# Optimization experiments

Hardware: AMD Instinct MI355X
Metric: run time of the kernel (lower is better)

## Reference

```python
import jax, jax.numpy as jnp
import numpy as np

B = 16384      # batch
H = 1024       # latent_dim
C = 2          # output_dim (classes)
PPC = 24       # prototypes per class
P = C * PPC    # 48 total prototypes
EPS = 1e-4


def setup_inputs() -> dict:
    key = jax.random.key(0)
    k1, k2, k3, k4, k5 = jax.random.split(key, 5)
    specific_user = jax.random.normal(k1, (B, H), jnp.float32)
    shared_user = jax.random.normal(k2, (B, H), jnp.float32)
    prototype_vectors = jax.random.normal(k3, (P, H), jnp.float32)
    # last_layer weight set by set_last_layer_incorrect_connection(-0.5):
    # +1 for the prototype's own class, -0.5 elsewhere; shape [C, P]
    cls = np.arange(P) // PPC
    ident = (cls[None, :] == np.arange(C)[:, None]).astype(np.float32)
    last_layer_w = jnp.asarray(ident * 1.0 + (1.0 - ident) * (-0.5))
    # nn.Bilinear(H, H, 1): weight [1, H, H], bias [1]
    bilinear_w = jax.random.normal(k4, (1, H, H), jnp.float32) / np.sqrt(H)
    bilinear_b = jax.random.normal(k5, (1,), jnp.float32) * 0.01
    return {
        "specific_user": specific_user,
        "shared_user": shared_user,
        "prototype_vectors": prototype_vectors,
        "last_layer_w": last_layer_w,
        "bilinear_w": bilinear_w,
        "bilinear_b": bilinear_b,
        "flag": 1,
    }


def reference(specific_user, shared_user, prototype_vectors, last_layer_w,
              bilinear_w, bilinear_b, flag):
    # prototype_distances: squared euclid via mm + norms, then log-similarity
    x2 = jnp.sum(specific_user ** 2, axis=1, keepdims=True)          # [B,1]
    p2 = jnp.sum(prototype_vectors ** 2, axis=1)                     # [P]
    distance = -2.0 * (specific_user @ prototype_vectors.T) + x2 + p2[None, :]  # [B,P]
    similarity = jnp.log((distance + 1.0) / (distance + EPS))        # [B,P]
    logits = similarity @ last_layer_w.T                             # [B,C]

    # select the class's 24 prototypes (flag picks class 1 or 0; static int)
    idx = 1 if flag else 0
    sub = prototype_vectors.reshape(C, PPC, H)[idx]                  # [PPC,H]

    # prototype_subgraph_distances: per original broadcast, each row of
    # all_sim is the batch-mean of the log-similarity -> constant over batch.
    s2 = jnp.sum(sub ** 2, axis=1)                                   # [PPC]
    d = -2.0 * (specific_user @ sub.T) + x2 + s2[None, :]            # [B,PPC]
    sim = jnp.mean(jnp.log((d + 1.0) / (d + EPS)), axis=0)           # [PPC]
    jstar = jnp.argmax(sim)                                          # scalar
    chosen_proto = jnp.broadcast_to(sub[jstar], specific_user.shape) # [B,H]

    # nn.Bilinear(chosen_proto, shared_user) -> [B,1]
    pos = jnp.einsum('bi,ij,bj->b', chosen_proto, bilinear_w[0], shared_user)[:, None] + bilinear_b
    return (pos, shared_user, logits, distance)
```

## Files before the change

kernel.cpp:

```cpp
#include <hip/hip_runtime.h>
#include <hip/hip_bf16.h>

#define BATCH 16384
#define HD    1024
#define NP    48
#define PPC   24
#define EPSV  1e-4f

typedef __attribute__((ext_vector_type(8))) short  short8;
typedef __attribute__((ext_vector_type(4))) float  floatx4;

__device__ __forceinline__ float b2f(unsigned short s) {
    union { unsigned u; float f; } c; c.u = ((unsigned)s) << 16; return c.f;
}
__device__ __forceinline__ unsigned short f2bu(float f) {
    __hip_bfloat16 h = __float2bfloat16(f);
    union { __hip_bfloat16 h; unsigned short u; } c; c.h = h; return c.u;
}

__global__ __launch_bounds__(256) void k_prep(const float* __restrict__ proto,
                                              unsigned short* __restrict__ phi,
                                              unsigned short* __restrict__ plo,
                                              float* __restrict__ p2,
                                              float* __restrict__ vzero,
                                              float* __restrict__ gcol) {
    const int p = blockIdx.x;
    const int tid = threadIdx.x;
    if (p < 4)                        vzero[p * 256 + tid] = 0.f;
    else if (p == 4 && tid < NP)      gcol[tid] = 0.f;

    const float* row = proto + (size_t)p * HD;
    float acc = 0.f;
#pragma unroll
    for (int c = 0; c < 4; ++c) {
        const int k = c * 256 + tid;
        const float f = row[k];
        acc += f * f;
        const unsigned short h = f2bu(f);
        phi[(size_t)p * HD + k] = h;
        plo[(size_t)p * HD + k] = f2bu(f - b2f(h));
    }
#pragma unroll
    for (int m = 32; m >= 1; m >>= 1) acc += __shfl_xor(acc, m, 64);
    __shared__ float wsum[4];
    if ((tid & 63) == 0) wsum[tid >> 6] = acc;
    __syncthreads();
    if (tid == 0) p2[p] = wsum[0] + wsum[1] + wsum[2] + wsum[3];
}

__global__ __launch_bounds__(256, 4) void k_mainA(
    const float* __restrict__ x,
    const unsigned short* __restrict__ phi,
    const unsigned short* __restrict__ plo,
    float* __restrict__ dotp,
    float* __restrict__ x2h)
{
    __shared__ float lacc[4][64][13];
    __shared__ float lx2[4][16];
    const int wave = threadIdx.x >> 6;
    const int lane = threadIdx.x & 63;
    const int quad = lane >> 4;
    const int lr   = lane & 15;
    const int band = blockIdx.x >> 1;
    const int kh   = blockIdx.x & 1;
    const int rb   = band * 16;
    const int ko   = kh * 512 + wave * 128;

    const float* xr = x + (size_t)(rb + lr) * HD + ko + quad * 8;
    const unsigned short* ph0 = phi + (size_t)lr * HD + ko + quad * 8;
    const unsigned short* ph1 = ph0 + 16 * HD;
    const unsigned short* ph2 = ph0 + 32 * HD;
    const unsigned short* pl0 = plo + (size_t)lr * HD + ko + quad * 8;
    const unsigned short* pl1 = pl0 + 16 * HD;
    const unsigned short* pl2 = pl0 + 32 * HD;

    floatx4 acc0 = {0.f, 0.f, 0.f, 0.f};
    floatx4 acc1 = {0.f, 0.f, 0.f, 0.f};
    floatx4 acc2 = {0.f, 0.f, 0.f, 0.f};
    float x2p = 0.f;

#pragma unroll 2
    for (int kk = 0; kk < 4; ++kk) {
        const floatx4 xa = *(const floatx4*)(xr + kk * 32);
        const floatx4 xb = *(const floatx4*)(xr + kk * 32 + 4);
        short8 ah, al;
#pragma unroll
        for (int j = 0; j < 4; ++j) {
            const float f = xa[j];
            x2p += f * f;
            const unsigned short h = f2bu(f);
            ah[j] = (short)h;
            al[j] = (short)f2bu(f - b2f(h));
        }
#pragma unroll
        for (int j = 0; j < 4; ++j) {
            const float f = xb[j];
            x2p += f * f;
            const unsigned short h = f2bu(f);
            ah[4 + j] = (short)h;
            al[4 + j] = (short)f2bu(f - b2f(h));
        }
        const short8 bh0 = *(const short8*)(ph0 + kk * 32);
        const short8 bh1 = *(const short8*)(ph1 + kk * 32);
        const short8 bh2 = *(const short8*)(ph2 + kk * 32);
        const short8 bl0 = *(const short8*)(pl0 + kk * 32);
        const short8 bl1 = *(const short8*)(pl1 + kk * 32);
        const short8 bl2 = *(const short8*)(pl2 + kk * 32);
        acc0 = __builtin_amdgcn_mfma_f32_16x16x32_bf16(ah, bh0, acc0, 0, 0, 0);
        acc0 = __builtin_amdgcn_mfma_f32_16x16x32_bf16(ah, bl0, acc0, 0, 0, 0);
        acc0 = __builtin_amdgcn_mfma_f32_16x16x32_bf16(al, bh0, acc0, 0, 0, 0);
        acc1 = __builtin_amdgcn_mfma_f32_16x16x32_bf16(ah, bh1, acc1, 0, 0, 0);
        acc1 = __builtin_amdgcn_mfma_f32_16x16x32_bf16(ah, bl1, acc1, 0, 0, 0);
        acc1 = __builtin_amdgcn_mfma_f32_16x16x32_bf16(al, bh1, acc1, 0, 0, 0);
        acc2 = __builtin_amdgcn_mfma_f32_16x16x32_bf16(ah, bh2, acc2, 0, 0, 0);
        acc2 = __builtin_amdgcn_mfma_f32_16x16x32_bf16(ah, bl2, acc2, 0, 0, 0);
        acc2 = __builtin_amdgcn_mfma_f32_16x16x32_bf16(al, bh2, acc2, 0, 0, 0);
    }
    x2p += __shfl_xor(x2p, 16, 64);
    x2p += __shfl_xor(x2p, 32, 64);

#pragma unroll
    for (int r = 0; r < 4; ++r) {
        lacc[wave][lane][r]     = acc0[r];
        lacc[wave][lane][4 + r] = acc1[r];
        lacc[wave][lane][8 + r] = acc2[r];
    }
    if (quad == 0) lx2[wave][lr] = x2p;
    __syncthreads();
    if (wave != 0) return;

    float facc[12];
#pragma unroll
    for (int i = 0; i < 12; ++i)
        facc[i] = lacc[0][lane][i] + lacc[1][lane][i] + lacc[2][lane][i] + lacc[3][lane][i];
    const float x2full = lx2[0][lr] + lx2[1][lr] + lx2[2][lr] + lx2[3][lr];

    float* drow = dotp + ((size_t)kh * 1024 + band) * (16 * NP);
#pragma unroll
    for (int t = 0; t < 3; ++t)
#pragma unroll
        for (int r = 0; r < 4; ++r)
            drow[(quad * 4 + r) * NP + t * 16 + lr] = facc[t * 4 + r];
    if (quad == 0) x2h[((size_t)kh * 1024 + band) * 16 + lr] = x2full;
}

__global__ __launch_bounds__(256) void k_fin(
    const float* __restrict__ dotp,
    const float* __restrict__ x2h,
    const float* __restrict__ p2,
    const float* __restrict__ llw,
    float* __restrict__ gcol,
    float* __restrict__ out_logits,
    float* __restrict__ out_dist)
{
    __shared__ float gsum[NP];
    const int wave = threadIdx.x >> 6;
    const int lane = threadIdx.x & 63;
    const int band = blockIdx.x;
    if (threadIdx.x < NP) gsum[threadIdx.x] = 0.f;
    __syncthreads();

    const float p2p = (lane < NP) ? p2[lane] : 0.f;
    const float w0  = (lane < NP) ? llw[lane] : 0.f;
    const float w1  = (lane < NP) ? llw[NP + lane] : 0.f;
    const float* dA = dotp + (size_t)band * (16 * NP);
    const float* dB = dotp + ((size_t)1024 + band) * (16 * NP);
    float csum = 0.f;

#pragma unroll
    for (int r = 0; r < 4; ++r) {
        const int rrow = wave * 4 + r;
        const int row  = band * 16 + rrow;
        const float x2 = x2h[band * 16 + rrow] + x2h[1024 * 16 + band * 16 + rrow];
        float sim = 0.f;
        if (lane < NP) {
            const float dot = dA[rrow * NP + lane] + dB[rrow * NP + lane];
            const float d = -2.f * dot + x2 + p2p;
            out_dist[(size_t)row * NP + lane] = d;
            sim = log1pf((1.f - EPSV) / (d + EPSV));
        }
        csum += sim;
        float r0 = sim * w0, r1 = sim * w1;
#pragma unroll
        for (int m = 1; m <= 32; m <<= 1) {
            r0 += __shfl_xor(r0, m, 64);
            r1 += __shfl_xor(r1, m, 64);
        }
        if (lane == 0) {
            out_logits[(size_t)row * 2 + 0] = r0;
            out_logits[(size_t)row * 2 + 1] = r1;
        }
    }
    if (lane < NP) atomicAdd(&gsum[lane], csum);
    __syncthreads();
    if (threadIdx.x < NP) atomicAdd(&gcol[threadIdx.x], gsum[threadIdx.x]);
}

__global__ __launch_bounds__(256, 4) void k_main_fb(
    const float* __restrict__ x,
    const unsigned short* __restrict__ phi,
    const unsigned short* __restrict__ plo,
    const float* __restrict__ llw,
    const float* __restrict__ p2,
    float* __restrict__ gcol,
    float* __restrict__ out_logits,
    float* __restrict__ out_dist)
{
    __shared__ float lacc[4][64][13];
    __shared__ float lx2[4][16];
    const int wave = threadIdx.x >> 6;
    const int lane = threadIdx.x & 63;
    const int quad = lane >> 4;
    const int lr   = lane & 15;
    const int rb   = blockIdx.x * 16;
    const int ko   = wave * 256;

    const float* xr = x + (size_t)(rb + lr) * HD + ko + quad * 8;
    const unsigned short* ph0 = phi + (size_t)lr * HD + ko + quad * 8;
    const unsigned short* ph1 = ph0 + 16 * HD;
    const unsigned short* ph2 = ph0 + 32 * HD;
    const unsigned short* pl0 = plo + (size_t)lr * HD + ko + quad * 8;
    const unsigned short* pl1 = pl0 + 16 * HD;
    const unsigned short* pl2 = pl0 + 32 * HD;

    floatx4 acc0 = {0.f, 0.f, 0.f, 0.f};
    floatx4 acc1 = {0.f, 0.f, 0.f, 0.f};
    floatx4 acc2 = {0.f, 0.f, 0.f, 0.f};
    float x2p = 0.f;

#pragma unroll 2
    for (int kk = 0; kk < 8; ++kk) {
        const floatx4 xa = *(const floatx4*)(xr + kk * 32);
        const floatx4 xb = *(const floatx4*)(xr + kk * 32 + 4);
        short8 ah, al;
#pragma unroll
        for (int j = 0; j < 4; ++j) {
            const float f = xa[j];
            x2p += f * f;
            const unsigned short h = f2bu(f);
            ah[j] = (short)h;
            al[j] = (short)f2bu(f - b2f(h));
        }
#pragma unroll
        for (int j = 0; j < 4; ++j) {
            const float f = xb[j];
            x2p += f * f;
            const unsigned short h = f2bu(f);
            ah[4 + j] = (short)h;
            al[4 + j] = (short)f2bu(f - b2f(h));
        }
        const short8 bh0 = *(const short8*)(ph0 + kk * 32);
        const short8 bh1 = *(const short8*)(ph1 + kk * 32);
        const short8 bh2 = *(const short8*)(ph2 + kk * 32);
        const short8 bl0 = *(const short8*)(pl0 + kk * 32);
        const short8 bl1 = *(const short8*)(pl1 + kk * 32);
        const short8 bl2 = *(const short8*)(pl2 + kk * 32);
        acc0 = __builtin_amdgcn_mfma_f32_16x16x32_bf16(ah, bh0, acc0, 0, 0, 0);
        acc0 = __builtin_amdgcn_mfma_f32_16x16x32_bf16(ah, bl0, acc0, 0, 0, 0);
        acc0 = __builtin_amdgcn_mfma_f32_16x16x32_bf16(al, bh0, acc0, 0, 0, 0);
        acc1 = __builtin_amdgcn_mfma_f32_16x16x32_bf16(ah, bh1, acc1, 0, 0, 0);
        acc1 = __builtin_amdgcn_mfma_f32_16x16x32_bf16(ah, bl1, acc1, 0, 0, 0);
        acc1 = __builtin_amdgcn_mfma_f32_16x16x32_bf16(al, bh1, acc1, 0, 0, 0);
        acc2 = __builtin_amdgcn_mfma_f32_16x16x32_bf16(ah, bh2, acc2, 0, 0, 0);
        acc2 = __builtin_amdgcn_mfma_f32_16x16x32_bf16(ah, bl2, acc2, 0, 0, 0);
        acc2 = __builtin_amdgcn_mfma_f32_16x16x32_bf16(al, bh2, acc2, 0, 0, 0);
    }
    x2p += __shfl_xor(x2p, 16, 64);
    x2p += __shfl_xor(x2p, 32, 64);

#pragma unroll
    for (int r = 0; r < 4; ++r) {
        lacc[wave][lane][r]     = acc0[r];
        lacc[wave][lane][4 + r] = acc1[r];
        lacc[wave][lane][8 + r] = acc2[r];
    }
    if (quad == 0) lx2[wave][lr] = x2p;
    __syncthreads();
    if (wave != 0) return;

    float facc[12];
#pragma unroll
    for (int i = 0; i < 12; ++i)
        facc[i] = lacc[0][lane][i] + lacc[1][lane][i] + lacc[2][lane][i] + lacc[3][lane][i];
    const float x2full = lx2[0][lr] + lx2[1][lr] + lx2[2][lr] + lx2[3][lr];

    float s0[4] = {0.f, 0.f, 0.f, 0.f};
    float s1[4] = {0.f, 0.f, 0.f, 0.f};

#pragma unroll
    for (int t = 0; t < 3; ++t) {
        const int p = t * 16 + lr;
        const float p2p = p2[p];
        const float w0 = llw[p];
        const float w1 = llw[NP + p];
        float cst = 0.f;
#pragma unroll
        for (int r = 0; r < 4; ++r) {
            const int row = quad * 4 + r;
            const float x2r = __shfl(x2full, row, 64);
            const float d = -2.f * facc[t * 4 + r] + x2r + p2p;
            out_dist[(size_t)(rb + row) * NP + p] = d;
            const float sim = log1pf((1.f - EPSV) / (d + EPSV));
            s0[r] += sim * w0;
            s1[r] += sim * w1;
            cst += sim;
        }
        cst += __shfl_xor(cst, 16, 64);
        cst += __shfl_xor(cst, 32, 64);
        if (quad == 0) atomicAdd(&gcol[p], cst);
    }

#pragma unroll
    for (int r = 0; r < 4; ++r) {
        float r0 = s0[r], r1 = s1[r];
#pragma unroll
        for (int m = 1; m <= 8; m <<= 1) {
            r0 += __shfl_xor(r0, m, 64);
            r1 += __shfl_xor(r1, m, 64);
        }
        if (lr == 0) {
            const int brow = rb + quad * 4 + r;
            out_logits[(size_t)brow * 2 + 0] = r0;
            out_logits[(size_t)brow * 2 + 1] = r1;
        }
    }
}

__global__ __launch_bounds__(256) void k_matvec(
    const float* __restrict__ proto,
    const float* __restrict__ w2,
    const float* __restrict__ gcol,
    const int* __restrict__ flag,
    float* __restrict__ v)
{
    __shared__ int js;
    const int tid = threadIdx.x;
    const int idx = (flag[0] != 0) ? 1 : 0;
    if (tid == 0) {
        const float* cs = gcol + idx * PPC;
        int bj = 0; float bv = cs[0];
        for (int j = 1; j < PPC; ++j)
            if (cs[j] > bv) { bv = cs[j]; bj = j; }
        js = bj;
    }
    __syncthreads();

    const float* crow = proto + (size_t)(idx * PPC + js) * HD;
    const int i0 = blockIdx.x * 16;
    const int j4 = tid * 4;
    float a0 = 0.f, a1 = 0.f, a2 = 0.f, a3 = 0.f;
#pragma unroll 4
    for (int i = i0; i < i0 + 16; ++i) {
        const float c = crow[i];
        const floatx4 wv = *(const floatx4*)(w2 + (size_t)i * HD + j4);
        a0 += c * wv[0];
        a1 += c * wv[1];
        a2 += c * wv[2];
        a3 += c * wv[3];
    }
    atomicAdd(&v[j4 + 0], a0);
    atomicAdd(&v[j4 + 1], a1);
    atomicAdd(&v[j4 + 2], a2);
    atomicAdd(&v[j4 + 3], a3);
}

__global__ __launch_bounds__(256) void k_pos(
    const float* __restrict__ sh,
    const float* __restrict__ v,
    const float* __restrict__ bias,
    float* __restrict__ out_pos,
    float* __restrict__ out_copy)
{
    const int wave = threadIdx.x >> 6;
    const int lane = threadIdx.x & 63;
    const int b = blockIdx.x * 4 + wave;

    const floatx4* src = (const floatx4*)(sh + (size_t)b * HD);
    floatx4* dst = (floatx4*)(out_copy + (size_t)b * HD);
    const floatx4* vv = (const floatx4*)v;
    float acc = 0.f;
#pragma unroll
    for (int c = 0; c < 4; ++c) {
        const int idx = c * 64 + lane;
        const floatx4 r = src[idx];
        __builtin_nontemporal_store(r, &dst[idx]);
        const floatx4 vr = vv[idx];
#pragma unroll
        for (int j = 0; j < 4; ++j) acc += r[j] * vr[j];
    }
#pragma unroll
    for (int m = 1; m <= 32; m <<= 1) acc += __shfl_xor(acc, m, 64);
    if (lane == 0) out_pos[b] = acc + bias[0];
}

extern "C" void kernel_launch(void* const* d_in, const int* in_sizes, int n_in,
                              void* d_out, int out_size, void* d_ws, size_t ws_size,
                              hipStream_t stream) {
    const float* x     = (const float*)d_in[0];
    const float* sh    = (const float*)d_in[1];
    const float* proto = (const float*)d_in[2];
    const float* llw   = (const float*)d_in[3];
    const float* w2    = (const float*)d_in[4];
    const float* bb    = (const float*)d_in[5];
    const int*   flag  = (const int*)d_in[6];

    float* out = (float*)d_out;
    float* out_pos    = out;
    float* out_copy   = out + BATCH;
    float* out_logits = out + BATCH + BATCH * HD;
    float* out_dist   = out + BATCH + BATCH * HD + BATCH * 2;

    float* ws_v    = (float*)d_ws;
    float* ws_col  = ws_v + 1024;
    float* ws_p2   = ws_v + 1088;
    unsigned short* ws_phi = (unsigned short*)(ws_v + 16384);
    unsigned short* ws_plo = ws_phi + NP * HD;
    float* ws_dot  = ws_v + 65536;
    float* ws_x2   = ws_v + 1638400;
    const bool big_ws = ws_size >= (size_t)1671168 * 4;

    k_prep<<<48, 256, 0, stream>>>(proto, ws_phi, ws_plo, ws_p2, ws_v, ws_col);
    if (big_ws) {
        k_mainA<<<2048, 256, 0, stream>>>(x, ws_phi, ws_plo, ws_dot, ws_x2);
        k_fin<<<1024, 256, 0, stream>>>(ws_dot, ws_x2, ws_p2, llw, ws_col, out_logits, out_dist);
    } else {
        k_main_fb<<<1024, 256, 0, stream>>>(x, ws_phi, ws_plo, llw, ws_p2, ws_col, out_logits, out_dist);
    }
    k_matvec<<<64, 256, 0, stream>>>(proto, w2, ws_col, flag, ws_v);
    k_pos<<<4096, 256, 0, stream>>>(sh, ws_v, bb, out_pos, out_copy);
}
```

Baseline: 236.4 us.

## Fuse all stages into one persistent cooperative kernel with grid syncs

```diff
diff --git a/kernel.cpp b/kernel.cpp
--- a/kernel.cpp
+++ b/kernel.cpp
@@ -1,5 +1,8 @@
 #include <hip/hip_runtime.h>
 #include <hip/hip_bf16.h>
+#include <hip/hip_cooperative_groups.h>
+
+namespace cg = cooperative_groups;
 
 #define BATCH 16384
 #define HD    1024
@@ -16,6 +19,246 @@
 __device__ __forceinline__ unsigned short f2bu(float f) {
     __hip_bfloat16 h = __float2bfloat16(f);
     union { __hip_bfloat16 h; unsigned short u; } c; c.h = h; return c.u;
+}
+
+__global__ __launch_bounds__(256, 4) void k_fused(
+    const float* __restrict__ x,
+    const float* __restrict__ sh,
+    const float* __restrict__ proto,
+    const float* __restrict__ llw,
+    const float* __restrict__ w2,
+    const float* __restrict__ bb,
+    const int*   __restrict__ flag,
+    float* __restrict__ out_pos,
+    float* __restrict__ out_copy,
+    float* __restrict__ out_logits,
+    float* __restrict__ out_dist,
+    unsigned short* __restrict__ phi,
+    unsigned short* __restrict__ plo,
+    float* __restrict__ p2,
+    float* __restrict__ v,
+    float* __restrict__ gcol,
+    float* __restrict__ dotp,
+    float* __restrict__ x2h)
+{
+    __shared__ float lacc[4][64][13];
+    __shared__ float lx2[4][16];
+    __shared__ float gsum[NP];
+    __shared__ float wsum[4];
+    __shared__ int   js;
+
+    cg::grid_group grid = cg::this_grid();
+    const int bid  = blockIdx.x;
+    const int G    = gridDim.x;
+    const int tid  = threadIdx.x;
+    const int wave = tid >> 6;
+    const int lane = tid & 63;
+    const int quad = lane >> 4;
+    const int lr   = lane & 15;
+
+    for (int p = bid; p < 48; p += G) {
+        if (p < 4)                   v[p * 256 + tid] = 0.f;
+        else if (p == 4 && tid < NP) gcol[tid] = 0.f;
+        const float* row = proto + (size_t)p * HD;
+        float acc = 0.f;
+#pragma unroll
+        for (int c = 0; c < 4; ++c) {
+            const int k = c * 256 + tid;
+            const float f = row[k];
+            acc += f * f;
+            const unsigned short h = f2bu(f);
+            phi[(size_t)p * HD + k] = h;
+            plo[(size_t)p * HD + k] = f2bu(f - b2f(h));
+        }
+#pragma unroll
+        for (int m = 32; m >= 1; m >>= 1) acc += __shfl_xor(acc, m, 64);
+        if (lane == 0) wsum[wave] = acc;
+        __syncthreads();
+        if (tid == 0) p2[p] = wsum[0] + wsum[1] + wsum[2] + wsum[3];
+        __syncthreads();
+    }
+    grid.sync();
+
+    for (int vb = bid; vb < 2048; vb += G) {
+        const int band = vb >> 1;
+        const int kh   = vb & 1;
+        const int rb   = band * 16;
+        const int ko   = kh * 512 + wave * 128;
+
+        const float* xr = x + (size_t)(rb + lr) * HD + ko + quad * 8;
+        const unsigned short* ph0 = phi + (size_t)lr * HD + ko + quad * 8;
+        const unsigned short* ph1 = ph0 + 16 * HD;
+        const unsigned short* ph2 = ph0 + 32 * HD;
+        const unsigned short* pl0 = plo + (size_t)lr * HD + ko + quad * 8;
+        const unsigned short* pl1 = pl0 + 16 * HD;
+        const unsigned short* pl2 = pl0 + 32 * HD;
+
+        floatx4 acc0 = {0.f, 0.f, 0.f, 0.f};
+        floatx4 acc1 = {0.f, 0.f, 0.f, 0.f};
+        floatx4 acc2 = {0.f, 0.f, 0.f, 0.f};
+        float x2p = 0.f;
+
+#pragma unroll 2
+        for (int kk = 0; kk < 4; ++kk) {
+            const floatx4 xa = *(const floatx4*)(xr + kk * 32);
+            const floatx4 xb = *(const floatx4*)(xr + kk * 32 + 4);
+            short8 ah, al;
+#pragma unroll
+            for (int j = 0; j < 4; ++j) {
+                const float f = xa[j];
+                x2p += f * f;
+                const unsigned short h = f2bu(f);
+                ah[j] = (short)h;
+                al[j] = (short)f2bu(f - b2f(h));
+            }
+#pragma unroll
+            for (int j = 0; j < 4; ++j) {
+                const float f = xb[j];
+                x2p += f * f;
+                const unsigned short h = f2bu(f);
+                ah[4 + j] = (short)h;
+                al[4 + j] = (short)f2bu(f - b2f(h));
+            }
+            const short8 bh0 = *(const short8*)(ph0 + kk * 32);
+            const short8 bh1 = *(const short8*)(ph1 + kk * 32);
+            const short8 bh2 = *(const short8*)(ph2 + kk * 32);
+            const short8 bl0 = *(const short8*)(pl0 + kk * 32);
+            const short8 bl1 = *(const short8*)(pl1 + kk * 32);
+            const short8 bl2 = *(const short8*)(pl2 + kk * 32);
+            acc0 = __builtin_amdgcn_mfma_f32_16x16x32_bf16(ah, bh0, acc0, 0, 0, 0);
+            acc0 = __builtin_amdgcn_mfma_f32_16x16x32_bf16(ah, bl0, acc0, 0, 0, 0);
+            acc0 = __builtin_amdgcn_mfma_f32_16x16x32_bf16(al, bh0, acc0, 0, 0, 0);
+            acc1 = __builtin_amdgcn_mfma_f32_16x16x32_bf16(ah, bh1, acc1, 0, 0, 0);
+            acc1 = __builtin_amdgcn_mfma_f32_16x16x32_bf16(ah, bl1, acc1, 0, 0, 0);
+            acc1 = __builtin_amdgcn_mfma_f32_16x16x32_bf16(al, bh1, acc1, 0, 0, 0);
+            acc2 = __builtin_amdgcn_mfma_f32_16x16x32_bf16(ah, bh2, acc2, 0, 0, 0);
+            acc2 = __builtin_amdgcn_mfma_f32_16x16x32_bf16(ah, bl2, acc2, 0, 0, 0);
+            acc2 = __builtin_amdgcn_mfma_f32_16x16x32_bf16(al, bh2, acc2, 0, 0, 0);
+        }
+        x2p += __shfl_xor(x2p, 16, 64);
+        x2p += __shfl_xor(x2p, 32, 64);
+
+#pragma unroll
+        for (int r = 0; r < 4; ++r) {
+            lacc[wave][lane][r]     = acc0[r];
+            lacc[wave][lane][4 + r] = acc1[r];
+            lacc[wave][lane][8 + r] = acc2[r];
+        }
+        if (quad == 0) lx2[wave][lr] = x2p;
+        __syncthreads();
+        if (wave == 0) {
+            float facc[12];
+#pragma unroll
+            for (int i = 0; i < 12; ++i)
+                facc[i] = lacc[0][lane][i] + lacc[1][lane][i] + lacc[2][lane][i] + lacc[3][lane][i];
+            const float x2full = lx2[0][lr] + lx2[1][lr] + lx2[2][lr] + lx2[3][lr];
+
+            float* drow = dotp + ((size_t)kh * 1024 + band) * (16 * NP);
+#pragma unroll
+            for (int t = 0; t < 3; ++t)
+#pragma unroll
+                for (int r = 0; r < 4; ++r)
+                    drow[(quad * 4 + r) * NP + t * 16 + lr] = facc[t * 4 + r];
+            if (quad == 0) x2h[((size_t)kh * 1024 + band) * 16 + lr] = x2full;
+        }
+        __syncthreads();
+    }
+    grid.sync();
+
+    for (int band = bid; band < 1024; band += G) {
+        if (tid < NP) gsum[tid] = 0.f;
+        __syncthreads();
+
+        const float p2p = (lane < NP) ? p2[lane] : 0.f;
+        const float w0  = (lane < NP) ? llw[lane] : 0.f;
+        const float w1  = (lane < NP) ? llw[NP + lane] : 0.f;
+        const float* dA = dotp + (size_t)band * (16 * NP);
+        const float* dB = dotp + ((size_t)1024 + band) * (16 * NP);
+        float csum = 0.f;
+
+#pragma unroll
+        for (int r = 0; r < 4; ++r) {
+            const int rrow = wave * 4 + r;
+            const int row  = band * 16 + rrow;
+            const float x2 = x2h[band * 16 + rrow] + x2h[1024 * 16 + band * 16 + rrow];
+            float sim = 0.f;
+            if (lane < NP) {
+                const float dot = dA[rrow * NP + lane] + dB[rrow * NP + lane];
+                const float d = -2.f * dot + x2 + p2p;
+                out_dist[(size_t)row * NP + lane] = d;
+                sim = log1pf((1.f - EPSV) / (d + EPSV));
+            }
+            csum += sim;
+            float r0 = sim * w0, r1 = sim * w1;
+#pragma unroll
+            for (int m = 1; m <= 32; m <<= 1) {
+                r0 += __shfl_xor(r0, m, 64);
+                r1 += __shfl_xor(r1, m, 64);
+            }
+            if (lane == 0) {
+                out_logits[(size_t)row * 2 + 0] = r0;
+                out_logits[(size_t)row * 2 + 1] = r1;
+            }
+        }
+        if (lane < NP) atomicAdd(&gsum[lane], csum);
+        __syncthreads();
+        if (tid < NP) atomicAdd(&gcol[tid], gsum[tid]);
+        __syncthreads();
+    }
+    grid.sync();
+
+    {
+        const int idx = (flag[0] != 0) ? 1 : 0;
+        for (int vb = bid; vb < 256; vb += G) {
+            if (tid == 0) {
+                const float* cs = gcol + idx * PPC;
+                int bj = 0; float bv = cs[0];
+                for (int j = 1; j < PPC; ++j)
+                    if (cs[j] > bv) { bv = cs[j]; bj = j; }
+                js = bj;
+            }
+            __syncthreads();
+            const float* crow = proto + (size_t)(idx * PPC + js) * HD;
+            const int i0 = vb * 4;
+            const int j4 = tid * 4;
+            float a0 = 0.f, a1 = 0.f, a2 = 0.f, a3 = 0.f;
+#pragma unroll
+            for (int i = i0; i < i0 + 4; ++i) {
+                const float c = crow[i];
+                const floatx4 wv = *(const floatx4*)(w2 + (size_t)i * HD + j4);
+                a0 += c * wv[0];
+                a1 += c * wv[1];
+                a2 += c * wv[2];
+                a3 += c * wv[3];
+            }
+            atomicAdd(&v[j4 + 0], a0);
+            atomicAdd(&v[j4 + 1], a1);
+            atomicAdd(&v[j4 + 2], a2);
+            atomicAdd(&v[j4 + 3], a3);
+            __syncthreads();
+        }
+    }
+    grid.sync();
+
+    for (int vb = bid; vb < 4096; vb += G) {
+        const int b = vb * 4 + wave;
+        const floatx4* src = (const floatx4*)(sh + (size_t)b * HD);
+        floatx4* dst = (floatx4*)(out_copy + (size_t)b * HD);
+        const floatx4* vv = (const floatx4*)v;
+        float acc = 0.f;
+#pragma unroll
+        for (int c = 0; c < 4; ++c) {
+            const int idx2 = c * 64 + lane;
+            const floatx4 r = src[idx2];
+            __builtin_nontemporal_store(r, &dst[idx2]);
+            const floatx4 vr = vv[idx2];
+#pragma unroll
+            for (int j = 0; j < 4; ++j) acc += r[j] * vr[j];
+        }
+#pragma unroll
+        for (int m = 1; m <= 32; m <<= 1) acc += __shfl_xor(acc, m, 64);
+        if (lane == 0) out_pos[b] = acc + bb[0];
+    }
 }
 
 __global__ __launch_bounds__(256) void k_prep(const float* __restrict__ proto,
@@ -46,154 +289,6 @@
     if ((tid & 63) == 0) wsum[tid >> 6] = acc;
     __syncthreads();
     if (tid == 0) p2[p] = wsum[0] + wsum[1] + wsum[2] + wsum[3];
-}
-
-__global__ __launch_bounds__(256, 4) void k_mainA(
-    const float* __restrict__ x,
-    const unsigned short* __restrict__ phi,
-    const unsigned short* __restrict__ plo,
-    float* __restrict__ dotp,
-    float* __restrict__ x2h)
-{
-    __shared__ float lacc[4][64][13];
-    __shared__ float lx2[4][16];
-    const int wave = threadIdx.x >> 6;
-    const int lane = threadIdx.x & 63;
-    const int quad = lane >> 4;
-    const int lr   = lane & 15;
-    const int band = blockIdx.x >> 1;
-    const int kh   = blockIdx.x & 1;
-    const int rb   = band * 16;
-    const int ko   = kh * 512 + wave * 128;
-
-    const float* xr = x + (size_t)(rb + lr) * HD + ko + quad * 8;
-    const unsigned short* ph0 = phi + (size_t)lr * HD + ko + quad * 8;
-    const unsigned short* ph1 = ph0 + 16 * HD;
-    const unsigned short* ph2 = ph0 + 32 * HD;
-    const unsigned short* pl0 = plo + (size_t)lr * HD + ko + quad * 8;
-    const unsigned short* pl1 = pl0 + 16 * HD;
-    const unsigned short* pl2 = pl0 + 32 * HD;
-
-    floatx4 acc0 = {0.f, 0.f, 0.f, 0.f};
-    floatx4 acc1 = {0.f, 0.f, 0.f, 0.f};
-    floatx4 acc2 = {0.f, 0.f, 0.f, 0.f};
-    float x2p = 0.f;
-
-#pragma unroll 2
-    for (int kk = 0; kk < 4; ++kk) {
-        const floatx4 xa = *(const floatx4*)(xr + kk * 32);
-        const floatx4 xb = *(const floatx4*)(xr + kk * 32 + 4);
-        short8 ah, al;
-#pragma unroll
-        for (int j = 0; j < 4; ++j) {
-            const float f = xa[j];
-            x2p += f * f;
-            const unsigned short h = f2bu(f);
-            ah[j] = (short)h;
-            al[j] = (short)f2bu(f - b2f(h));
-        }
-#pragma unroll
-        for (int j = 0; j < 4; ++j) {
-            const float f = xb[j];
-            x2p += f * f;
-            const unsigned short h = f2bu(f);
-            ah[4 + j] = (short)h;
-            al[4 + j] = (short)f2bu(f - b2f(h));
-        }
-        const short8 bh0 = *(const short8*)(ph0 + kk * 32);
-        const short8 bh1 = *(const short8*)(ph1 + kk * 32);
-        const short8 bh2 = *(const short8*)(ph2 + kk * 32);
-        const short8 bl0 = *(const short8*)(pl0 + kk * 32);
-        const short8 bl1 = *(const short8*)(pl1 + kk * 32);
-        const short8 bl2 = *(const short8*)(pl2 + kk * 32);
-        acc0 = __builtin_amdgcn_mfma_f32_16x16x32_bf16(ah, bh0, acc0, 0, 0, 0);
-        acc0 = __builtin_amdgcn_mfma_f32_16x16x32_bf16(ah, bl0, acc0, 0, 0, 0);
-        acc0 = __builtin_amdgcn_mfma_f32_16x16x32_bf16(al, bh0, acc0, 0, 0, 0);
-        acc1 = __builtin_amdgcn_mfma_f32_16x16x32_bf16(ah, bh1, acc1, 0, 0, 0);
-        acc1 = __builtin_amdgcn_mfma_f32_16x16x32_bf16(ah, bl1, acc1, 0, 0, 0);
-        acc1 = __builtin_amdgcn_mfma_f32_16x16x32_bf16(al, bh1, acc1, 0, 0, 0);
-        acc2 = __builtin_amdgcn_mfma_f32_16x16x32_bf16(ah, bh2, acc2, 0, 0, 0);
-        acc2 = __builtin_amdgcn_mfma_f32_16x16x32_bf16(ah, bl2, acc2, 0, 0, 0);
-        acc2 = __builtin_amdgcn_mfma_f32_16x16x32_bf16(al, bh2, acc2, 0, 0, 0);
-    }
-    x2p += __shfl_xor(x2p, 16, 64);
-    x2p += __shfl_xor(x2p, 32, 64);
-
-#pragma unroll
-    for (int r = 0; r < 4; ++r) {
-        lacc[wave][lane][r]     = acc0[r];
-        lacc[wave][lane][4 + r] = acc1[r];
-        lacc[wave][lane][8 + r] = acc2[r];
-    }
-    if (quad == 0) lx2[wave][lr] = x2p;
-    __syncthreads();
-    if (wave != 0) return;
-
-    float facc[12];
-#pragma unroll
-    for (int i = 0; i < 12; ++i)
-        facc[i] = lacc[0][lane][i] + lacc[1][lane][i] + lacc[2][lane][i] + lacc[3][lane][i];
-    const float x2full = lx2[0][lr] + lx2[1][lr] + lx2[2][lr] + lx2[3][lr];
-
-    float* drow = dotp + ((size_t)kh * 1024 + band) * (16 * NP);
-#pragma unroll
-    for (int t = 0; t < 3; ++t)
-#pragma unroll
-        for (int r = 0; r < 4; ++r)
-            drow[(quad * 4 + r) * NP + t * 16 + lr] = facc[t * 4 + r];
-    if (quad == 0) x2h[((size_t)kh * 1024 + band) * 16 + lr] = x2full;
-}
-
-__global__ __launch_bounds__(256) void k_fin(
-    const float* __restrict__ dotp,
-    const float* __restrict__ x2h,
-    const float* __restrict__ p2,
-    const float* __restrict__ llw,
-    float* __restrict__ gcol,
-    float* __restrict__ out_logits,
-    float* __restrict__ out_dist)
-{
-    __shared__ float gsum[NP];
-    const int wave = threadIdx.x >> 6;
-    const int lane = threadIdx.x & 63;
-    const int band = blockIdx.x;
-    if (threadIdx.x < NP) gsum[threadIdx.x] = 0.f;
-    __syncthreads();
-
-    const float p2p = (lane < NP) ? p2[lane] : 0.f;
-    const float w0  = (lane < NP) ? llw[lane] : 0.f;
-    const float w1  = (lane < NP) ? llw[NP + lane] : 0.f;
-    const float* dA = dotp + (size_t)band * (16 * NP);
-    const float* dB = dotp + ((size_t)1024 + band) * (16 * NP);
-    float csum = 0.f;
-
-#pragma unroll
-    for (int r = 0; r < 4; ++r) {
-        const int rrow = wave * 4 + r;
-        const int row  = band * 16 + rrow;
-        const float x2 = x2h[band * 16 + rrow] + x2h[1024 * 16 + band * 16 + rrow];
-        float sim = 0.f;
-        if (lane < NP) {
-            const float dot = dA[rrow * NP + lane] + dB[rrow * NP + lane];
-            const float d = -2.f * dot + x2 + p2p;
-            out_dist[(size_t)row * NP + lane] = d;
-            sim = log1pf((1.f - EPSV) / (d + EPSV));
-        }
-        csum += sim;
-        float r0 = sim * w0, r1 = sim * w1;
-#pragma unroll
-        for (int m = 1; m <= 32; m <<= 1) {
-            r0 += __shfl_xor(r0, m, 64);
-            r1 += __shfl_xor(r1, m, 64);
-        }
-        if (lane == 0) {
-            out_logits[(size_t)row * 2 + 0] = r0;
-            out_logits[(size_t)row * 2 + 1] = r1;
-        }
-    }
-    if (lane < NP) atomicAdd(&gsum[lane], csum);
-    __syncthreads();
-    if (threadIdx.x < NP) atomicAdd(&gcol[threadIdx.x], gsum[threadIdx.x]);
 }
 
 __global__ __launch_bounds__(256, 4) void k_main_fb(
@@ -419,13 +514,34 @@
     float* ws_x2   = ws_v + 1638400;
     const bool big_ws = ws_size >= (size_t)1671168 * 4;
 
-    k_prep<<<48, 256, 0, stream>>>(proto, ws_phi, ws_plo, ws_p2, ws_v, ws_col);
+    bool launched = false;
     if (big_ws) {
-        k_mainA<<<2048, 256, 0, stream>>>(x, ws_phi, ws_plo, ws_dot, ws_x2);
-        k_fin<<<1024, 256, 0, stream>>>(ws_dot, ws_x2, ws_p2, llw, ws_col, out_logits, out_dist);
-    } else {
+        static int coop_grid = 0;
+        if (coop_grid == 0) {
+            int nb = 0;
+            if (hipOccupancyMaxActiveBlocksPerMultiprocessor(&nb, k_fused, 256, 0) != hipSuccess || nb < 1)
+                nb = 0;
+            long g = (long)nb * 256;
+            if (g > 2048) g = 2048;
+            coop_grid = (int)g;
+        }
+        if (coop_grid >= 256) {
+            void* args[] = {
+                (void*)&x, (void*)&sh, (void*)&proto, (void*)&llw, (void*)&w2,
+                (void*)&bb, (void*)&flag, (void*)&out_pos, (void*)&out_copy,
+                (void*)&out_logits, (void*)&out_dist, (void*)&ws_phi,
+                (void*)&ws_plo, (void*)&ws_p2, (void*)&ws_v, (void*)&ws_col,
+                (void*)&ws_dot, (void*)&ws_x2 };
+            hipError_t e = hipLaunchCooperativeKernel(
+                (void*)k_fused, dim3(coop_grid), dim3(256), args, 0, stream);
+            launched = (e == hipSuccess);
+        }
+    }
+
+    if (!launched) {
+        k_prep<<<48, 256, 0, stream>>>(proto, ws_phi, ws_plo, ws_p2, ws_v, ws_col);
         k_main_fb<<<1024, 256, 0, stream>>>(x, ws_phi, ws_plo, llw, ws_p2, ws_col, out_logits, out_dist);
-    }
-    k_matvec<<<64, 256, 0, stream>>>(proto, w2, ws_col, flag, ws_v);
-    k_pos<<<4096, 256, 0, stream>>>(sh, ws_v, bb, out_pos, out_copy);
-}
+        k_matvec<<<64, 256, 0, stream>>>(proto, w2, ws_col, flag, ws_v);
+        k_pos<<<4096, 256, 0, stream>>>(sh, ws_v, bb, out_pos, out_copy);
+    }
+}
```

Result: slower. 441.5 us (+86.8%).
